# Optimization experiments

Measured on AMD Instinct MI355X. Metric: run time of the kernel, lower is better.

Reference implementation:

```python
import jax, jax.numpy as jnp
import numpy as np

B, S, E = 2, 2048, 2048
H, KVH, D = 16, 4, 128
GROUPS = H // KVH
WINDOW = 1024
CAP = 50.0
ROPE_BASE = 10000.0
RMS_EPS = 1e-6
LN_EPS = 1e-5

def setup_inputs() -> dict:
    key = jax.random.key(0)
    ks = jax.random.split(key, 5)
    return {
        "x": jax.random.normal(ks[0], (B, S, E), jnp.float32),
        "Wq": jax.random.normal(ks[1], (E, E), jnp.float32) * (1.0 / np.sqrt(E)),
        "Wk": jax.random.normal(ks[2], (KVH * D, E), jnp.float32) * (1.0 / np.sqrt(E)),
        "Wv": jax.random.normal(ks[3], (KVH * D, E), jnp.float32) * (1.0 / np.sqrt(E)),
        "Wo": jax.random.normal(ks[4], (E, E), jnp.float32) * (1.0 / np.sqrt(E * H)),
        "q_norm_w": jnp.ones((D,), jnp.float32),
        "k_norm_w": jnp.ones((D,), jnp.float32),
        "ln_gamma": jnp.ones((E,), jnp.float32),
        "ln_beta": jnp.zeros((E,), jnp.float32),
    }

def _rmsnorm(t, w):
    # normalize over last (head) dim
    var = jnp.mean(jnp.square(t), axis=-1, keepdims=True)
    return t * jax.lax.rsqrt(var + RMS_EPS) * w

def _rope(t):
    # t: [B, h, S, D]; rotate-half RoPE
    half = D // 2
    inv_freq = 1.0 / (ROPE_BASE ** (jnp.arange(0, D, 2, dtype=jnp.float32) / D))  # [D/2]
    ang = jnp.arange(S, dtype=jnp.float32)[:, None] * inv_freq[None, :]  # [S, D/2]
    cos = jnp.concatenate([jnp.cos(ang), jnp.cos(ang)], axis=-1)  # [S, D]
    sin = jnp.concatenate([jnp.sin(ang), jnp.sin(ang)], axis=-1)
    t1, t2 = t[..., :half], t[..., half:]
    rot = jnp.concatenate([-t2, t1], axis=-1)
    return t * cos + rot * sin

def reference(x, Wq, Wk, Wv, Wo, q_norm_w, k_norm_w, ln_gamma, ln_beta):
    b, s, _ = x.shape
    q = (x @ Wq.T).reshape(b, s, H, D).transpose(0, 2, 1, 3)    # [B,H,S,D]
    k = (x @ Wk.T).reshape(b, s, KVH, D).transpose(0, 2, 1, 3)  # [B,KVH,S,D]
    v = (x @ Wv.T).reshape(b, s, KVH, D).transpose(0, 2, 1, 3)
    # QK-RMSNorm (Gemma/PaLM2 style), then RoPE
    q = _rope(_rmsnorm(q, q_norm_w))
    k = _rope(_rmsnorm(k, k_norm_w))
    # GQA: repeat KV heads to match query heads
    k = jnp.repeat(k, GROUPS, axis=1)  # [B,H,S,D]
    v = jnp.repeat(v, GROUPS, axis=1)
    scores = jnp.einsum('bhqd,bhkd->bhqk', q, k) / jnp.sqrt(jnp.asarray(D, x.dtype))
    # tanh logit softcap (Gemma2)
    scores = CAP * jnp.tanh(scores / CAP)
    # causal + sliding-window mask: attend to j with 0 <= i-j < WINDOW
    i = jnp.arange(s)[:, None]
    j = jnp.arange(s)[None, :]
    mask = (j <= i) & ((i - j) < WINDOW)  # [S,S]
    neg = jnp.finfo(scores.dtype).min
    scores = jnp.where(mask[None, None], scores, neg)
    attn = jax.nn.softmax(scores, axis=-1)
    out = jnp.einsum('bhqk,bhkd->bhqd', attn, v)  # [B,H,S,D]
    out = out.transpose(0, 2, 1, 3).reshape(b, s, E) @ Wo.T
    # residual + LayerNorm (post-norm)
    y = x + out
    mu = jnp.mean(y, axis=-1, keepdims=True)
    var = jnp.var(y, axis=-1, keepdims=True)
    return (y - mu) * jax.lax.rsqrt(var + LN_EPS) * ln_gamma + ln_beta
```

## Files before the change

### kernel.cpp

```cpp
#include <hip/hip_runtime.h>
#include <stdint.h>

typedef __attribute__((ext_vector_type(8))) short short8;
typedef __attribute__((ext_vector_type(4))) float f32x4;
typedef unsigned short u16;
typedef unsigned int u32;

#define NTOK 4096
#define E 2048
#define S 2048
#define NH 16
#define NKVH 4
#define HD 128
#define NQKV 3072

__device__ __forceinline__ float bf2f(u16 u) {
    return __uint_as_float(((u32)u) << 16);
}
__device__ __forceinline__ u16 f2bf(float f) {
    u32 u = __float_as_uint(f);
    u32 r = (u + 0x7fffu + ((u >> 16) & 1u)) >> 16;
    return (u16)r;
}
__device__ __forceinline__ void gload_lds16(const u16* g, u16* l) {
    __builtin_amdgcn_global_load_lds(
        (const __attribute__((address_space(1))) unsigned int*)(g),
        (__attribute__((address_space(3))) unsigned int*)(l), 16, 0, 0);
}

__global__ void cast5(const float* __restrict__ x, const float* __restrict__ wq,
                      const float* __restrict__ wk, const float* __restrict__ wv,
                      const float* __restrict__ wo,
                      u16* __restrict__ xb, u16* __restrict__ wqkvb,
                      u16* __restrict__ wob) {
    int i = blockIdx.x * 256 + threadIdx.x;
    const float* s; u16* d; int rel;
    if (i < 2097152)      { s = x;  d = xb;  rel = i; }
    else if (i < 3145728) { s = wq; d = wqkvb; rel = i - 2097152; }
    else if (i < 3407872) { s = wk; d = wqkvb + 4194304; rel = i - 3145728; }
    else if (i < 3670016) { s = wv; d = wqkvb + 5242880; rel = i - 3407872; }
    else                  { s = wo; d = wob; rel = i - 3670016; }
    float4 v = *(const float4*)(s + (size_t)rel * 4);
    ushort4 o;
    o.x = f2bf(v.x); o.y = f2bf(v.y); o.z = f2bf(v.z); o.w = f2bf(v.w);
    *(ushort4*)(d + (size_t)rel * 4) = o;
}

#define LADDR(row, ko) ((row) * 64 + ((ko) ^ (((row) & 7) << 3)))

__device__ __forceinline__ void stageA(u16* lds, const u16* g, int ldsrow0,
                                       int g0, int g1, int kt, int K, int tid) {
    const int rr = tid >> 3;
    const int chunk = (tid & 7) ^ (rr & 7);
    const int w8 = (tid >> 6) * 8;
    gload_lds16(g + (size_t)(g0 + rr) * K + kt + chunk * 8,
                lds + (ldsrow0 + w8) * 64);
    gload_lds16(g + (size_t)(g1 + rr) * K + kt + chunk * 8,
                lds + (ldsrow0 + 64 + w8) * 64);
}
__device__ __forceinline__ void stageB(u16* lds, const u16* g, int ldsrow0,
                                       int b0, int b1, int kt, int K, int tid) {
    const int rr = tid >> 3;
    const int grow = (rr & 31) | ((rr & 32) << 1);
    const int chunk = (tid & 7) ^ (rr & 7);
    const int w8 = (tid >> 6) * 8;
    gload_lds16(g + (size_t)(b0 + grow) * K + kt + chunk * 8,
                lds + (ldsrow0 + w8) * 64);
    gload_lds16(g + (size_t)(b1 + grow) * K + kt + chunk * 8,
                lds + (ldsrow0 + 64 + w8) * 64);
}

#define GSB   __builtin_amdgcn_sched_barrier(0)
#define GBAR  __builtin_amdgcn_s_barrier()
#define LGKM0 do { asm volatile("s_waitcnt lgkmcnt(0)" ::: "memory"); GSB; } while (0)
#define MIDBAR do { GSB; GBAR; LGKM0; } while (0)
#define ENDBAR do { __builtin_amdgcn_s_setprio(0); GSB; GBAR; } while (0)

__global__ __launch_bounds__(512, 2)
void gemm8p(const u16* __restrict__ A, const u16* __restrict__ Bt,
            float* __restrict__ C, int M, int N, int K, int ksz, int nsplit) {
    __shared__ u16 As[2 * 16384];
    __shared__ u16 Bs[2 * 16384];
    const int tid = threadIdx.x;
    const int w = tid >> 6, lane = tid & 63;
    const int lr = lane & 15, quad = lane >> 4;
    const int qo = quad * 8;
    const int wm = (w >> 2) * 128, wn = (w & 3) * 64;
    const int wmh = (w >> 2) * 64, wnq = (w & 3) * 32;

    const int nbx = N >> 8;
    int wg = blockIdx.x;
    {
        const int nwg = gridDim.x;
        const int q = nwg >> 3, r = nwg & 7;
        const int xcd = wg & 7, loc = wg >> 3;
        wg = (xcd < r ? xcd * (q + 1) : r * (q + 1) + (xcd - r) * q) + loc;
    }
    int split = 0;
    if (nsplit == 2) { split = wg & 1; wg >>= 1; }
    const int n0 = (wg % nbx) << 8;
    const int m0 = (wg / nbx) << 8;

    const u16* gA = A + (size_t)m0 * K + split * ksz;
    const u16* gB = Bt + (size_t)n0 * K + split * ksz;
    C += (size_t)split * M * N;
    const int nt = ksz >> 6;

    f32x4 acc[8][4];
#pragma unroll
    for (int mi = 0; mi < 8; mi++)
#pragma unroll
        for (int ni = 0; ni < 4; ni++)
            acc[mi][ni] = (f32x4){0.f, 0.f, 0.f, 0.f};

    short8 alo[4][2], ahi[4][2], blo[2][2], bhi[2][2];

    stageA(As, gA, 0, 0, 128, 0, K, tid);
    stageB(Bs, gB, 0, 0, 128, 0, K, tid);
    stageB(Bs, gB, 128, 32, 160, 0, K, tid);
    stageA(As, gA, 128, 64, 192, 0, K, tid);
    if (nt > 1) {
        stageA(As + 16384, gA, 0, 0, 128, 64, K, tid);
        stageB(Bs + 16384, gB, 0, 0, 128, 64, K, tid);
        stageB(Bs + 16384, gB, 128, 32, 160, 64, K, tid);
        asm volatile("s_waitcnt vmcnt(6)" ::: "memory");
    } else {
        asm volatile("s_waitcnt vmcnt(0)" ::: "memory");
    }
    GSB; GBAR;

    for (int t = 0; t < nt; ++t) {
        const int pb = t & 1;
        u16* Ap = As + pb * 16384;
        u16* Bp = Bs + pb * 16384;
        u16* An = As + (pb ^ 1) * 16384;
        const int kt1 = (t + 1) << 6, kt2 = (t + 2) << 6;

#pragma unroll
        for (int mi = 0; mi < 4; mi++)
#pragma unroll
            for (int kk = 0; kk < 2; kk++)
                alo[mi][kk] = *(const short8*)&Ap[LADDR(wmh + mi * 16 + lr, kk * 32 + qo)];
#pragma unroll
        for (int ni = 0; ni < 2; ni++)
#pragma unroll
            for (int kk = 0; kk < 2; kk++)
                blo[ni][kk] = *(const short8*)&Bp[LADDR(wnq + ni * 16 + lr, kk * 32 + qo)];
        if (t + 1 < nt) stageA(An, gA, 128, 64, 192, kt1, K, tid);
        MIDBAR;
        __builtin_amdgcn_s_setprio(1);
#pragma unroll
        for (int mi = 0; mi < 4; mi++)
#pragma unroll
            for (int ni = 0; ni < 2; ni++)
#pragma unroll
                for (int kk = 0; kk < 2; kk++)
                    acc[mi][ni] = __builtin_amdgcn_mfma_f32_16x16x32_bf16(
                        alo[mi][kk], blo[ni][kk], acc[mi][ni], 0, 0, 0);
        ENDBAR;

#pragma unroll
        for (int ni = 0; ni < 2; ni++)
#pragma unroll
            for (int kk = 0; kk < 2; kk++)
                bhi[ni][kk] = *(const short8*)&Bp[LADDR(128 + wnq + ni * 16 + lr, kk * 32 + qo)];
        if (t + 2 < nt) stageA(Ap, gA, 0, 0, 128, kt2, K, tid);
        MIDBAR;
        __builtin_amdgcn_s_setprio(1);
#pragma unroll
        for (int mi = 0; mi < 4; mi++)
#pragma unroll
            for (int ni = 0; ni < 2; ni++)
#pragma unroll
                for (int kk = 0; kk < 2; kk++)
                    acc[mi][ni + 2] = __builtin_amdgcn_mfma_f32_16x16x32_bf16(
                        alo[mi][kk], bhi[ni][kk], acc[mi][ni + 2], 0, 0, 0);
        ENDBAR;

#pragma unroll
        for (int mi = 0; mi < 4; mi++)
#pragma unroll
            for (int kk = 0; kk < 2; kk++)
                ahi[mi][kk] = *(const short8*)&Ap[LADDR(128 + wmh + mi * 16 + lr, kk * 32 + qo)];
        if (t + 2 < nt) stageB(Bp, gB, 0, 0, 128, kt2, K, tid);
        MIDBAR;
        __builtin_amdgcn_s_setprio(1);
#pragma unroll
        for (int mi = 0; mi < 4; mi++)
#pragma unroll
            for (int ni = 0; ni < 2; ni++)
#pragma unroll
                for (int kk = 0; kk < 2; kk++)
                    acc[mi + 4][ni + 2] = __builtin_amdgcn_mfma_f32_16x16x32_bf16(
                        ahi[mi][kk], bhi[ni][kk], acc[mi + 4][ni + 2], 0, 0, 0);
        ENDBAR;

        if (t + 2 < nt) stageB(Bp, gB, 128, 32, 160, kt2, K, tid);
        __builtin_amdgcn_s_setprio(1);
#pragma unroll
        for (int mi = 0; mi < 4; mi++)
#pragma unroll
            for (int ni = 0; ni < 2; ni++)
#pragma unroll
                for (int kk = 0; kk < 2; kk++)
                    acc[mi + 4][ni] = __builtin_amdgcn_mfma_f32_16x16x32_bf16(
                        ahi[mi][kk], blo[ni][kk], acc[mi + 4][ni], 0, 0, 0);
        __builtin_amdgcn_s_setprio(0);
        if (t + 2 >= nt) {
            asm volatile("s_waitcnt vmcnt(0)" ::: "memory");
        } else {
            asm volatile("s_waitcnt vmcnt(6)" ::: "memory");
        }
        GSB; GBAR;
    }

#pragma unroll
    for (int mi = 0; mi < 8; mi++)
#pragma unroll
        for (int ni = 0; ni < 4; ni++) {
            const int row = m0 + wm + mi * 16 + quad * 4;
            const int col = n0 + wn + ni * 16 + lr;
            f32x4 v = acc[mi][ni];
            C[(size_t)(row + 0) * N + col] = v[0];
            C[(size_t)(row + 1) * N + col] = v[1];
            C[(size_t)(row + 2) * N + col] = v[2];
            C[(size_t)(row + 3) * N + col] = v[3];
        }
}

#define LDT 65
#define RMSBLKS 20480
__global__ __launch_bounds__(256)
void prep(const float* __restrict__ qkv,
          const float* __restrict__ qw, const float* __restrict__ kw,
          u16* __restrict__ qdst, u16* __restrict__ kdst, u16* __restrict__ vdst) {
    __shared__ u16 Ts[128 * LDT];
    if (blockIdx.x < RMSBLKS) {
        int p = blockIdx.x * 4 + (threadIdx.x >> 6);
        int lane = threadIdx.x & 63;
        const float* src; const float* w; u16* dst; int HH;
        if (p < NTOK * NH) { src = qkv; w = qw; dst = qdst; HH = NH; }
        else { p -= NTOK * NH; src = qkv + 2048; w = kw; dst = kdst; HH = NKVH; }
        int n = p / HH;
        int h = p - n * HH;
        int b = n >> 11;
        int s = n & 2047;
        const float* row = src + (size_t)n * NQKV + h * HD;
        float t1 = row[lane];
        float t2 = row[lane + 64];
        float ss = t1 * t1 + t2 * t2;
#pragma unroll
        for (int o = 1; o < 64; o <<= 1) ss += __shfl_xor(ss, o);
        float r = rsqrtf(ss * (1.f / 128.f) + 1e-6f);
        float a1 = t1 * r * w[lane];
        float a2 = t2 * r * w[lane + 64];
        float freq = expf(lane * -0.14391156831212787f);
        float ang = (float)s * freq;
        float sn, cs;
        sincosf(ang, &sn, &cs);
        float o1 = a1 * cs - a2 * sn;
        float o2 = a2 * cs + a1 * sn;
        size_t base = (((size_t)(b * HH + h)) * S + s) * HD;
        dst[base + lane] = f2bf(o1);
        dst[base + 64 + lane] = f2bf(o2);
    } else {
        const int idx = blockIdx.x - RMSBLKS;
        const int t = threadIdx.x;
        const int s0 = (idx & 31) * 64;
        const int kh = (idx >> 5) & 3;
        const int b = idx >> 7;
        const float* base = qkv + ((size_t)(b * S + s0)) * NQKV + 2560 + kh * HD;
#pragma unroll
        for (int i = 0; i < 8; i++) {
            int ii = i * 256 + t;
            int r = ii >> 5, c4 = (ii & 31) * 4;
            float4 v = *(const float4*)(base + (size_t)r * NQKV + c4);
            Ts[(c4 + 0) * LDT + r] = f2bf(v.x);
            Ts[(c4 + 1) * LDT + r] = f2bf(v.y);
            Ts[(c4 + 2) * LDT + r] = f2bf(v.z);
            Ts[(c4 + 3) * LDT + r] = f2bf(v.w);
        }
        __syncthreads();
        u16* obase = vdst + ((size_t)(b * NKVH + kh) * HD) * S + s0;
#pragma unroll
        for (int i = 0; i < 4; i++) {
            int ii = i * 256 + t;
            int d = ii >> 3, s8 = (ii & 7) * 8;
            const u16* row = &Ts[d * LDT + s8];
            short8 o;
#pragma unroll
            for (int j = 0; j < 8; j++) o[j] = (short)row[j];
            *(short8*)(obase + (size_t)d * S + s8) = o;
        }
    }
}

#define KSX(key, cb) ((key) * 128 + ((((cb) ^ ((key) & 15))) * 8))
#define VSX(d, cb)   ((d) * 64 + ((((cb) ^ ((d) & 7))) * 8))
#define PSX(row, cb) ((row) * 64 + ((((cb) ^ ((row) & 7))) * 8))
#define QBLK 64

__global__ __launch_bounds__(256, 4)
void attn_mfma(const u16* __restrict__ qa, const u16* __restrict__ ka,
               const u16* __restrict__ vt, u16* __restrict__ out) {
    __shared__ u16 Ks[64 * 128];
    __shared__ u16 Vs[128 * 64];
    __shared__ u16 Ps[64 * 64];
    const int tid = threadIdx.x;
    const int w = tid >> 6, lane = tid & 63;
    const int lr = lane & 15, quad = lane >> 4;
    const int hb = blockIdx.x;
    const int h = hb >> 1, b = hb & 1;
    const int kh = h >> 2;
    const int qt = (int)(gridDim.y - 1) - blockIdx.y;
    const int q0 = qt * QBLK;
    const int qg0 = q0 + w * 16;

    const float KQK = 0.0051006974f;
    const float KP  = -144.26950408889634f;

    short8 qf[4];
    {
        const u16* qrow = qa + (((size_t)(b * NH + h)) * S + qg0 + lr) * HD;
#pragma unroll
        for (int c = 0; c < 4; c++)
            qf[c] = *(const short8*)(qrow + c * 32 + quad * 8);
    }

    f32x4 O[8];
#pragma unroll
    for (int dt = 0; dt < 8; dt++) O[dt] = (f32x4){0.f, 0.f, 0.f, 0.f};
    float l[4] = {0.f, 0.f, 0.f, 0.f};

    const u16* kbase0 = ka + (((size_t)(b * NKVH + kh)) * S) * HD;
    const u16* vtbase0 = vt + ((size_t)(b * NKVH + kh) * HD) * S;

    const int jt0 = (q0 >= 1024) ? (q0 - 1024) : 0;
    const int jtend = q0;
    const int qmin = qg0, qmax = qg0 + 15;

    for (int jt = jt0; jt <= jtend; jt += 64) {
        const u16* kbase = kbase0 + (size_t)jt * HD;
        const u16* vtbase = vtbase0 + jt;
        __syncthreads();
#pragma unroll
        for (int i = 0; i < 4; i++) {
            int idx = i * 256 + tid;
            int key = idx >> 4, cbk = (idx & 15) ^ (key & 15);
            gload_lds16(kbase + (size_t)key * HD + cbk * 8,
                        &Ks[(i * 256 + w * 64) * 8]);
            int dd = idx >> 3, cbv = (idx & 7) ^ (dd & 7);
            gload_lds16(vtbase + (size_t)dd * S + cbv * 8,
                        &Vs[(i * 256 + w * 64) * 8]);
        }
        __syncthreads();

        u16* Pw = &Ps[w * 16 * 64];
        bool any = false;

#pragma unroll
        for (int kt = 0; kt < 4; kt++) {
            const int keymin = jt + kt * 16;
            bool need = (keymin <= qmax) && (keymin + 15 >= qmin - 1023);
            bool full = (keymin + 15 <= qmin) && (keymin >= qmax - 1023);
            if (need) {
                any = true;
                f32x4 a = (f32x4){0.f, 0.f, 0.f, 0.f};
#pragma unroll
                for (int c = 0; c < 4; c++) {
                    short8 kf = *(const short8*)(&Ks[KSX(kt * 16 + lr, 4 * c + quad)]);
                    a = __builtin_amdgcn_mfma_f32_16x16x32_bf16(qf[c], kf, a, 0, 0, 0);
                }
#pragma unroll
                for (int r = 0; r < 4; r++) {
                    float t = __builtin_amdgcn_exp2f(a[r] * KQK);
                    float p = __builtin_amdgcn_exp2f(
                        KP * __builtin_amdgcn_rcpf(t + 1.f));
                    if (!full) {
                        int rel = keymin + lr - (qg0 + quad * 4 + r);
                        bool valid = (rel <= 0) && (rel > -1024);
                        p = valid ? p : 0.f;
                    }
                    l[r] += p;
                    Pw[PSX(quad * 4 + r, kt * 2 + (lr >> 3)) + (lr & 7)] =
                        (u16)(__float_as_uint(p) >> 16);
                }
            } else {
#pragma unroll
                for (int r = 0; r < 4; r++)
                    Pw[PSX(quad * 4 + r, kt * 2 + (lr >> 3)) + (lr & 7)] = 0;
            }
        }

        if (any) {
#pragma unroll
            for (int c2 = 0; c2 < 2; c2++) {
                short8 pf = *(const short8*)(&Pw[PSX(lr, c2 * 4 + quad)]);
#pragma unroll
                for (int dt = 0; dt < 8; dt++) {
                    short8 vf = *(const short8*)(&Vs[VSX(dt * 16 + lr, c2 * 4 + quad)]);
                    O[dt] = __builtin_amdgcn_mfma_f32_16x16x32_bf16(pf, vf, O[dt], 0, 0, 0);
                }
            }
        }
    }

#pragma unroll
    for (int r = 0; r < 4; r++) {
        l[r] += __shfl_xor(l[r], 1);
        l[r] += __shfl_xor(l[r], 2);
        l[r] += __shfl_xor(l[r], 4);
        l[r] += __shfl_xor(l[r], 8);
    }
#pragma unroll
    for (int r = 0; r < 4; r++) {
        float inv = 1.f / l[r];
        u16* orow = out + ((size_t)(b * S + qg0 + quad * 4 + r)) * E + h * HD;
#pragma unroll
        for (int dt = 0; dt < 8; dt++)
            orow[dt * 16 + lr] = f2bf(O[dt][r] * inv);
    }
}

__global__ __launch_bounds__(256)
void ln_kernel(const float* __restrict__ x, const float* __restrict__ pr,
               const float* __restrict__ pr2,
               const float* __restrict__ g, const float* __restrict__ be,
               float* __restrict__ out) {
    int n = blockIdx.x;
    int tid = threadIdx.x;
    const float* xr = x + (size_t)n * E;
    const float* p = pr + (size_t)n * E;
    const float* p2 = pr2 + (size_t)n * E;
    float y[8];
    float s = 0.f, ss = 0.f;
#pragma unroll
    for (int i = 0; i < 2; i++) {
        float4 a = *(const float4*)(xr + tid * 8 + i * 4);
        float4 b = *(const float4*)(p + tid * 8 + i * 4);
        float c = 0.f;
        float4 cc = *(const float4*)(p2 + tid * 8 + i * 4);
        (void)c;
        float v0 = a.x + b.x + cc.x, v1 = a.y + b.y + cc.y;
        float v2 = a.z + b.z + cc.z, v3 = a.w + b.w + cc.w;
        y[i * 4 + 0] = v0; y[i * 4 + 1] = v1; y[i * 4 + 2] = v2; y[i * 4 + 3] = v3;
        s += v0 + v1 + v2 + v3;
        ss += v0 * v0 + v1 * v1 + v2 * v2 + v3 * v3;
    }
#pragma unroll
    for (int o = 1; o < 64; o <<= 1) {
        s += __shfl_xor(s, o);
        ss += __shfl_xor(ss, o);
    }
    __shared__ float r0[4], r1[4];
    int w = tid >> 6;
    if ((tid & 63) == 0) { r0[w] = s; r1[w] = ss; }
    __syncthreads();
    s = r0[0] + r0[1] + r0[2] + r0[3];
    ss = r1[0] + r1[1] + r1[2] + r1[3];
    float mu = s * (1.f / 2048.f);
    float var = ss * (1.f / 2048.f) - mu * mu;
    float rs = rsqrtf(var + 1e-5f);
    float* orow = out + (size_t)n * E;
#pragma unroll
    for (int i = 0; i < 8; i++) {
        int c = tid * 8 + i;
        orow[c] = (y[i] - mu) * rs * g[c] + be[c];
    }
}

extern "C" void kernel_launch(void* const* d_in, const int* in_sizes, int n_in,
                              void* d_out, int out_size, void* d_ws, size_t ws_size,
                              hipStream_t stream) {
    (void)in_sizes; (void)n_in; (void)out_size; (void)ws_size;
    const float* x   = (const float*)d_in[0];
    const float* Wq  = (const float*)d_in[1];
    const float* Wk  = (const float*)d_in[2];
    const float* Wv  = (const float*)d_in[3];
    const float* Wo  = (const float*)d_in[4];
    const float* qnw = (const float*)d_in[5];
    const float* knw = (const float*)d_in[6];
    const float* lng = (const float*)d_in[7];
    const float* lnb = (const float*)d_in[8];
    float* out = (float*)d_out;

    char* ws = (char*)d_ws;
    size_t off = 0;
    auto alloc = [&](size_t bytes) -> char* {
        char* pp = ws + off;
        off = (off + bytes + 255) & ~(size_t)255;
        return pp;
    };
    u16*  xb     = (u16*)alloc((size_t)NTOK * E * 2);
    u16*  Wqkvb  = (u16*)alloc((size_t)NQKV * E * 2);
    u16*  Wob    = (u16*)alloc((size_t)E * E * 2);
    float* qkvraw= (float*)alloc((size_t)NTOK * NQKV * 4);
    u16*  qaa    = (u16*)alloc((size_t)NTOK * E * 2);
    u16*  kaa    = (u16*)alloc((size_t)NTOK * 512 * 2);
    u16*  vtt    = (u16*)alloc((size_t)NTOK * 512 * 2);
    u16*  attn_o = xb;
    float* proj  = qkvraw;

    cast5<<<dim3(18432), 256, 0, stream>>>(x, Wq, Wk, Wv, Wo, xb, Wqkvb, Wob);

    gemm8p<<<dim3((NTOK / 256) * (NQKV / 256)), 512, 0, stream>>>(
        xb, Wqkvb, qkvraw, NTOK, NQKV, E, E, 1);

    prep<<<dim3(RMSBLKS + 256), 256, 0, stream>>>(qkvraw, qnw, knw, qaa, kaa, vtt);

    attn_mfma<<<dim3(NH * 2, S / QBLK), 256, 0, stream>>>(qaa, kaa, vtt, attn_o);

    gemm8p<<<dim3((NTOK / 256) * (E / 256) * 2), 512, 0, stream>>>(
        attn_o, Wob, proj, NTOK, E, E, E / 2, 2);

    ln_kernel<<<dim3(NTOK), 256, 0, stream>>>(
        x, proj, proj + (size_t)NTOK * E, lng, lnb, out);
}
```

Baseline: 316.6 us.

## Add dedicated 128x384-tile QKV GEMM kernel with staged double-buffered pipeline

Replaces the generic 256x256-tile GEMM for the QKV projection with a new kernel using 128x384 tiles. The grid becomes exactly 256 workgroups, one wave on 256 CUs instead of 192 tiles. Loads are staged in pieces interleaved with the MFMA phases across two LDS buffers. The aim is better CU utilisation and load/compute overlap, at the cost of lower arithmetic intensity per tile and more complex pipelining with vmcnt bookkeeping.

```diff
diff --git a/kernel.cpp b/kernel.cpp
--- a/kernel.cpp
+++ b/kernel.cpp
@@ -47,6 +47,161 @@
 }
 
 #define LADDR(row, ko) ((row) * 64 + ((ko) ^ (((row) & 7) << 3)))
+#define GSB   __builtin_amdgcn_sched_barrier(0)
+#define GBAR  __builtin_amdgcn_s_barrier()
+#define LGKM0 do { asm volatile("s_waitcnt lgkmcnt(0)" ::: "memory"); GSB; } while (0)
+#define MIDBAR do { GSB; GBAR; LGKM0; } while (0)
+#define ENDBAR do { __builtin_amdgcn_s_setprio(0); GSB; GBAR; } while (0)
+
+__device__ __forceinline__ void stage1(u16* lds, const u16* g, int row0,
+                                       int kt, int K, int tid) {
+    const int rr = tid >> 3;
+    const int chunk = (tid & 7) ^ (rr & 7);
+    gload_lds16(g + (size_t)(row0 + rr) * K + kt + chunk * 8,
+                lds + (row0 + (tid >> 6) * 8) * 64);
+}
+
+__global__ __launch_bounds__(512, 2)
+void gemm_qkv(const u16* __restrict__ A, const u16* __restrict__ Bt,
+              float* __restrict__ C, int M, int N, int K) {
+    __shared__ u16 As2[2 * 8192];
+    __shared__ u16 Bs2[2 * 24576];
+    const int tid = threadIdx.x;
+    const int w = tid >> 6, lane = tid & 63;
+    const int lr = lane & 15, quad = lane >> 4;
+    const int qo = quad * 8;
+    const int wr = w >> 2, wc = w & 3;
+    const int am = wr * 64;
+    const int bn = wc * 96;
+
+    const int nbx = N / 384;
+    int wg = blockIdx.x;
+    {
+        const int nwg = gridDim.x;
+        const int q = nwg >> 3, r = nwg & 7;
+        const int xcd = wg & 7, loc = wg >> 3;
+        wg = (xcd < r ? xcd * (q + 1) : r * (q + 1) + (xcd - r) * q) + loc;
+    }
+    const int n0 = (wg % nbx) * 384;
+    const int m0 = (wg / nbx) * 128;
+
+    const u16* gA = A + (size_t)m0 * K;
+    const u16* gB = Bt + (size_t)n0 * K;
+    const int nt = K >> 6;
+
+    f32x4 acc[4][6];
+#pragma unroll
+    for (int mi = 0; mi < 4; mi++)
+#pragma unroll
+        for (int ni = 0; ni < 6; ni++)
+            acc[mi][ni] = (f32x4){0.f, 0.f, 0.f, 0.f};
+
+    short8 af[4][2], bf[6][2];
+
+    stage1(As2, gA, 0, 0, K, tid);
+    stage1(As2, gA, 64, 0, K, tid);
+#pragma unroll
+    for (int r = 0; r < 6; r++) stage1(Bs2, gB, r * 64, 0, K, tid);
+    if (nt > 1) {
+        stage1(As2 + 8192, gA, 0, 64, K, tid);
+        stage1(As2 + 8192, gA, 64, 64, K, tid);
+#pragma unroll
+        for (int r = 0; r < 4; r++) stage1(Bs2 + 24576, gB, r * 64, 64, K, tid);
+        asm volatile("s_waitcnt vmcnt(6)" ::: "memory");
+    } else {
+        asm volatile("s_waitcnt vmcnt(0)" ::: "memory");
+    }
+    GSB; GBAR;
+
+    for (int t = 0; t < nt; ++t) {
+        const int pb = t & 1;
+        u16* Ap = As2 + pb * 8192;
+        u16* Bp = Bs2 + pb * 24576;
+        u16* Bn = Bs2 + (pb ^ 1) * 24576;
+        const int kt1 = (t + 1) << 6, kt2 = (t + 2) << 6;
+
+#pragma unroll
+        for (int mi = 0; mi < 4; mi++)
+#pragma unroll
+            for (int kk = 0; kk < 2; kk++)
+                af[mi][kk] = *(const short8*)&Ap[LADDR(am + mi * 16 + lr, kk * 32 + qo)];
+#pragma unroll
+        for (int ni = 0; ni < 3; ni++)
+#pragma unroll
+            for (int kk = 0; kk < 2; kk++)
+                bf[ni][kk] = *(const short8*)&Bp[LADDR(bn + ni * 16 + lr, kk * 32 + qo)];
+        if (t + 1 < nt) {
+            stage1(Bn, gB, 256, kt1, K, tid);
+            stage1(Bn, gB, 320, kt1, K, tid);
+        }
+        MIDBAR;
+        __builtin_amdgcn_s_setprio(1);
+#pragma unroll
+        for (int mi = 0; mi < 2; mi++)
+#pragma unroll
+            for (int ni = 0; ni < 3; ni++)
+#pragma unroll
+                for (int kk = 0; kk < 2; kk++)
+                    acc[mi][ni] = __builtin_amdgcn_mfma_f32_16x16x32_bf16(
+                        af[mi][kk], bf[ni][kk], acc[mi][ni], 0, 0, 0);
+        ENDBAR;
+
+#pragma unroll
+        for (int ni = 3; ni < 6; ni++)
+#pragma unroll
+            for (int kk = 0; kk < 2; kk++)
+                bf[ni][kk] = *(const short8*)&Bp[LADDR(bn + ni * 16 + lr, kk * 32 + qo)];
+        if (t + 2 < nt) {
+            stage1(Ap, gA, 0, kt2, K, tid);
+            stage1(Ap, gA, 64, kt2, K, tid);
+        }
+        MIDBAR;
+        __builtin_amdgcn_s_setprio(1);
+#pragma unroll
+        for (int mi = 0; mi < 2; mi++)
+#pragma unroll
+            for (int ni = 3; ni < 6; ni++)
+#pragma unroll
+                for (int kk = 0; kk < 2; kk++)
+                    acc[mi][ni] = __builtin_amdgcn_mfma_f32_16x16x32_bf16(
+                        af[mi][kk], bf[ni][kk], acc[mi][ni], 0, 0, 0);
+        ENDBAR;
+
+        if (t + 2 < nt) {
+#pragma unroll
+            for (int r = 0; r < 4; r++) stage1(Bp, gB, r * 64, kt2, K, tid);
+        }
+        __builtin_amdgcn_s_setprio(1);
+#pragma unroll
+        for (int mi = 2; mi < 4; mi++)
+#pragma unroll
+            for (int ni = 0; ni < 6; ni++)
+#pragma unroll
+                for (int kk = 0; kk < 2; kk++)
+                    acc[mi][ni] = __builtin_amdgcn_mfma_f32_16x16x32_bf16(
+                        af[mi][kk], bf[ni][kk], acc[mi][ni], 0, 0, 0);
+        __builtin_amdgcn_s_setprio(0);
+        if (t + 2 >= nt) {
+            asm volatile("s_waitcnt vmcnt(0)" ::: "memory");
+        } else {
+            asm volatile("s_waitcnt vmcnt(6)" ::: "memory");
+        }
+        GSB; GBAR;
+    }
+
+#pragma unroll
+    for (int mi = 0; mi < 4; mi++)
+#pragma unroll
+        for (int ni = 0; ni < 6; ni++) {
+            const int row = m0 + am + mi * 16 + quad * 4;
+            const int col = n0 + bn + ni * 16 + lr;
+            f32x4 v = acc[mi][ni];
+            C[(size_t)(row + 0) * N + col] = v[0];
+            C[(size_t)(row + 1) * N + col] = v[1];
+            C[(size_t)(row + 2) * N + col] = v[2];
+            C[(size_t)(row + 3) * N + col] = v[3];
+        }
+}
 
 __device__ __forceinline__ void stageA(u16* lds, const u16* g, int ldsrow0,
                                        int g0, int g1, int kt, int K, int tid) {
@@ -69,12 +224,6 @@
     gload_lds16(g + (size_t)(b1 + grow) * K + kt + chunk * 8,
                 lds + (ldsrow0 + 64 + w8) * 64);
 }
-
-#define GSB   __builtin_amdgcn_sched_barrier(0)
-#define GBAR  __builtin_amdgcn_s_barrier()
-#define LGKM0 do { asm volatile("s_waitcnt lgkmcnt(0)" ::: "memory"); GSB; } while (0)
-#define MIDBAR do { GSB; GBAR; LGKM0; } while (0)
-#define ENDBAR do { __builtin_amdgcn_s_setprio(0); GSB; GBAR; } while (0)
 
 __global__ __launch_bounds__(512, 2)
 void gemm8p(const u16* __restrict__ A, const u16* __restrict__ Bt,
@@ -438,9 +587,7 @@
     for (int i = 0; i < 2; i++) {
         float4 a = *(const float4*)(xr + tid * 8 + i * 4);
         float4 b = *(const float4*)(p + tid * 8 + i * 4);
-        float c = 0.f;
         float4 cc = *(const float4*)(p2 + tid * 8 + i * 4);
-        (void)c;
         float v0 = a.x + b.x + cc.x, v1 = a.y + b.y + cc.y;
         float v2 = a.z + b.z + cc.z, v3 = a.w + b.w + cc.w;
         y[i * 4 + 0] = v0; y[i * 4 + 1] = v1; y[i * 4 + 2] = v2; y[i * 4 + 3] = v3;
@@ -503,8 +650,7 @@
 
     cast5<<<dim3(18432), 256, 0, stream>>>(x, Wq, Wk, Wv, Wo, xb, Wqkvb, Wob);
 
-    gemm8p<<<dim3((NTOK / 256) * (NQKV / 256)), 512, 0, stream>>>(
-        xb, Wqkvb, qkvraw, NTOK, NQKV, E, E, 1);
+    gemm_qkv<<<dim3(256), 512, 0, stream>>>(xb, Wqkvb, qkvraw, NTOK, NQKV, E);
 
     prep<<<dim3(RMSBLKS + 256), 256, 0, stream>>>(qkvraw, qnw, knw, qaa, kaa, vtt);
 
```

After: 308.9 us. 2.4% less time.
